# Kernel optimization log

Measured on AMD Instinct MI355X. Metric: run time of the kernel, lower is better.

Reference implementation:

```python
import jax, jax.numpy as jnp
import numpy as np

B, N, D, H, FF, K, L = 8, 4096, 128, 8, 512, 16, 2
DH = D // H
EPS = 1e-5


def setup_inputs() -> dict:
    key = jax.random.key(0)
    ks = jax.random.split(key, 32)
    s = 0.02
    inp = {
        "x": jax.random.normal(ks[0], (B, N, 8), dtype=jnp.float32),
        "xyz_w": jax.random.normal(ks[1], (D, 3), jnp.float32) * s,
        "xyz_b": jnp.zeros((D,), jnp.float32),
        "ohe_w": jax.random.normal(ks[2], (D, 5), jnp.float32) * s,
        "ohe_b": jnp.zeros((D,), jnp.float32),
        # per-layer transformer params stacked on leading L axis
        "in_proj_w": jax.random.normal(ks[3], (L, 3 * D, D), jnp.float32) * s,
        "in_proj_b": jnp.zeros((L, 3 * D), jnp.float32),
        "out_proj_w": jax.random.normal(ks[4], (L, D, D), jnp.float32) * s,
        "out_proj_b": jnp.zeros((L, D), jnp.float32),
        "ln1_w": jnp.ones((L, D), jnp.float32),
        "ln1_b": jnp.zeros((L, D), jnp.float32),
        "lin1_w": jax.random.normal(ks[5], (L, FF, D), jnp.float32) * s,
        "lin1_b": jnp.zeros((L, FF), jnp.float32),
        "lin2_w": jax.random.normal(ks[6], (L, D, FF), jnp.float32) * s,
        "lin2_b": jnp.zeros((L, D), jnp.float32),
        "ln2_w": jnp.ones((L, D), jnp.float32),
        "ln2_b": jnp.zeros((L, D), jnp.float32),
        "fc1_w": jax.random.normal(ks[7], (FF, D), jnp.float32) * s,
        "fc1_b": jnp.zeros((FF,), jnp.float32),
        "fc2_w": jax.random.normal(ks[8], (1, FF), jnp.float32) * s,
        "fc2_b": jnp.zeros((1,), jnp.float32),
    }
    return inp


def _layer_norm(x, w, b):
    m = jnp.mean(x, -1, keepdims=True)
    v = jnp.mean((x - m) ** 2, -1, keepdims=True)
    return (x - m) * jax.lax.rsqrt(v + EPS) * w + b


def _knn_attention(xyz, feat):
    # squared euclidean distances preserve top-k ordering of cdist(p=2)
    d2 = jnp.sum((xyz[:, :, None, :] - xyz[:, None, :, :]) ** 2, -1)  # [B,N,N]
    _, idx = jax.lax.top_k(-d2, K + 1)  # ascending distance
    idx = idx[..., 1:]  # drop self -> [B,N,K]
    knn = jax.vmap(lambda f, i: f[i])(feat, idx)  # [B,N,K,D]
    scale = 1.0 / np.sqrt(D)
    scores = jnp.einsum('bnd,bnkd->bnk', feat, knn) * scale
    w = jax.nn.softmax(scores, -1)
    return jnp.einsum('bnk,bnkd->bnd', w, knn)


def _mha(x, in_w, in_b, out_w, out_b):
    qkv = x @ in_w.T + in_b  # [B,N,3D]
    q, k, v = jnp.split(qkv, 3, axis=-1)
    def heads(t):
        return t.reshape(B, N, H, DH).transpose(0, 2, 1, 3)  # [B,H,N,DH]
    q, k, v = heads(q), heads(k), heads(v)
    scores = jnp.einsum('bhqd,bhkd->bhqk', q, k) / np.sqrt(DH)
    a = jax.nn.softmax(scores, -1)
    o = jnp.einsum('bhqk,bhkd->bhqd', a, v).transpose(0, 2, 1, 3).reshape(B, N, D)
    return o @ out_w.T + out_b


def reference(x, xyz_w, xyz_b, ohe_w, ohe_b, in_proj_w, in_proj_b, out_proj_w,
              out_proj_b, ln1_w, ln1_b, lin1_w, lin1_b, lin2_w, lin2_b,
              ln2_w, ln2_b, fc1_w, fc1_b, fc2_w, fc2_b):
    xyz = x[:, :, :3]
    ohe = x[:, :, 3:8]
    feat = (xyz @ xyz_w.T + xyz_b) + (ohe @ ohe_w.T + ohe_b)  # [B,N,D]
    h = _knn_attention(xyz, feat)
    # post-norm TransformerEncoder (PyTorch default, relu, no dropout at eval)
    for l in range(L):
        a = _mha(h, in_proj_w[l], in_proj_b[l], out_proj_w[l], out_proj_b[l])
        h = _layer_norm(h + a, ln1_w[l], ln1_b[l])
        f = jax.nn.relu(h @ lin1_w[l].T + lin1_b[l]) @ lin2_w[l].T + lin2_b[l]
        h = _layer_norm(h + f, ln2_w[l], ln2_b[l])
    pooled = jnp.mean(h, axis=1)  # [B,D]
    out = jax.nn.sigmoid(jax.nn.relu(pooled @ fc1_w.T + fc1_b) @ fc2_w.T + fc2_b)
    return out
```

## Files before the change

kernel.cpp:

```cpp
#include <hip/hip_runtime.h>

#define Bq 8
#define Nq 4096
#define Dq 128
#define Hq 8
#define FFq 512
#define KNNq 16
#define Lq 2
#define DHq 16
#define EPSq 1e-5f

typedef _Float16 half4 __attribute__((ext_vector_type(4)));
typedef _Float16 half2t __attribute__((ext_vector_type(2)));
typedef float v4f __attribute__((ext_vector_type(4)));

static __device__ __forceinline__ half2t pkrtz(float a, float b) {
    return __builtin_bit_cast(half2t, __builtin_amdgcn_cvt_pkrtz(a, b));
}

__global__ void wcvt_kernel(const float* __restrict__ ipw, const float* __restrict__ opw,
                            const float* __restrict__ l1w, const float* __restrict__ l2w,
                            _Float16* __restrict__ wb) {
    int i = blockIdx.x * 256 + threadIdx.x;
    float v;
    if (i < 98304) v = ipw[i];
    else if (i < 131072) v = opw[i - 98304];
    else if (i < 262144) v = l1w[i - 131072];
    else v = l2w[i - 262144];
    wb[i] = (_Float16)v;
}

__global__ void feat_kernel(const float* __restrict__ x, const float* __restrict__ xyz_w,
                            const float* __restrict__ xyz_b, const float* __restrict__ ohe_w,
                            const float* __restrict__ ohe_b, float* __restrict__ feat) {
    int i = blockIdx.x * blockDim.x + threadIdx.x;
    if (i >= Bq * Nq * Dq) return;
    int d = i & 127;
    int t = i >> 7;
    const float* xr = x + (size_t)t * 8;
    float s = xyz_b[d] + ohe_b[d];
    s += xr[0] * xyz_w[d * 3 + 0] + xr[1] * xyz_w[d * 3 + 1] + xr[2] * xyz_w[d * 3 + 2];
    s += xr[3] * ohe_w[d * 5 + 0] + xr[4] * ohe_w[d * 5 + 1] + xr[5] * ohe_w[d * 5 + 2]
       + xr[6] * ohe_w[d * 5 + 3] + xr[7] * ohe_w[d * 5 + 4];
    feat[i] = s;
}

__global__ __launch_bounds__(256) void knn_kernel(const float* __restrict__ x, int* __restrict__ idx) {
    __shared__ __attribute__((aligned(16))) float sxyz[Nq][4];
    __shared__ unsigned int md[256][16];
    int b = blockIdx.y;
    int tid = threadIdx.x;
    for (int p = tid; p < Nq; p += 256) {
        const float* xr = x + ((size_t)b * Nq + p) * 8;
        float4 v = make_float4(xr[0], xr[1], xr[2], 0.f);
        *(float4*)&sxyz[p][0] = v;
    }
    __syncthreads();
    int qi = tid >> 3;
    int part = tid & 7;
    int n = blockIdx.x * 32 + qi;
    float qx = sxyz[n][0], qy = sxyz[n][1], qz = sxyz[n][2];
    unsigned int bd[KNNq];
#pragma unroll
    for (int i = 0; i < KNNq; i++) bd[i] = 0xFFFFFFFFu;
    int j0 = part * 512;
    int rot = part * 2;
#pragma unroll 2
    for (int jj = 0; jj < 512; jj++) {
        int j = j0 + ((jj + rot) & 511);
        float4 p4 = *(const float4*)&sxyz[j][0];
        float dx = qx - p4.x, dy = qy - p4.y, dz = qz - p4.z;
        float d2 = fmaf(dx, dx, fmaf(dy, dy, dz * dz));
        unsigned int key = (__float_as_uint(d2) & 0xFFFFF000u) | (unsigned int)j;
        key = (j == n) ? 0xFFFFFFFFu : key;
#pragma unroll
        for (int i = 0; i < KNNq; i++) {
            unsigned int lo = bd[i] < key ? bd[i] : key;
            unsigned int hi = bd[i] < key ? key : bd[i];
            bd[i] = lo; key = hi;
        }
    }
#pragma unroll
    for (int i = 0; i < KNNq; i++) md[tid][i] = bd[i];
    __syncthreads();
    if (part == 0) {
        unsigned int pall = 0;
        int* op = idx + ((size_t)b * Nq + n) * KNNq;
        int base_row = qi * 8;
#pragma unroll
        for (int s = 0; s < KNNq; s++) {
            unsigned int best = 0xFFFFFFFFu; int bp = 0;
#pragma unroll
            for (int p2 = 0; p2 < 8; p2++) {
                unsigned int ptr = (pall >> (p2 * 4)) & 15u;
                unsigned int v = md[base_row + p2][ptr];
                if (v < best) { best = v; bp = p2; }
            }
            op[s] = (int)(best & 4095u);
            pall += (1u << (bp * 4));
        }
    }
}

__global__ __launch_bounds__(256, 4) void knn_attn_kernel(const float* __restrict__ feat,
                                                          const int* __restrict__ idx,
                                                          float* __restrict__ h,
                                                          _Float16* __restrict__ h16) {
    int wave = threadIdx.x >> 6;
    int lane = threadIdx.x & 63;
    int token = blockIdx.x * 4 + wave;
    int b = token >> 12;
    const float2* frow = (const float2*)(feat + (size_t)token * Dq);
    float2 f = frow[lane];
    const int* ip = idx + (size_t)token * KNNq;
    int jj[KNNq];
#pragma unroll
    for (int k = 0; k < KNNq; k++) jj[k] = ip[k];
    float2 g[KNNq];
#pragma unroll
    for (int k = 0; k < KNNq; k++)
        g[k] = ((const float2*)(feat + (((size_t)b << 12) + jj[k]) * Dq))[lane];
    float sc[KNNq];
#pragma unroll
    for (int k = 0; k < KNNq; k++) {
        float p = f.x * g[k].x + f.y * g[k].y;
#pragma unroll
        for (int m = 1; m < 64; m <<= 1) p += __shfl_xor(p, m);
        sc[k] = p * 0.088388347648318447f;
    }
    float mx = sc[0];
#pragma unroll
    for (int k = 1; k < KNNq; k++) mx = fmaxf(mx, sc[k]);
    float sum = 0.f;
#pragma unroll
    for (int k = 0; k < KNNq; k++) { sc[k] = __expf(sc[k] - mx); sum += sc[k]; }
    float inv = 1.f / sum;
    float o0 = 0.f, o1 = 0.f;
#pragma unroll
    for (int k = 0; k < KNNq; k++) { o0 += sc[k] * g[k].x; o1 += sc[k] * g[k].y; }
    o0 *= inv; o1 *= inv;
    ((float2*)(h + (size_t)token * Dq))[lane] = make_float2(o0, o1);
    ((half2t*)(h16 + (size_t)token * Dq))[lane] = pkrtz(o0, o1);
}

template <int MODE>
__global__ __launch_bounds__(256) void hgemm_kernel(const _Float16* __restrict__ A,
                                                    const _Float16* __restrict__ W,
                                                    const float* __restrict__ bias,
                                                    void* __restrict__ Cout,
                                                    int M, int Nc, int K) {
    int tid = threadIdx.x;
    int lane = tid & 63, w = tid >> 6;
    int l15 = lane & 15, l4 = lane >> 4;
    int m0 = blockIdx.y * 64 + w * 16;
    int n0 = blockIdx.x * 64;
    const _Float16* Ap = A + (size_t)(m0 + l15) * K + l4 * 4;
    const _Float16* Wp = W + (size_t)(n0 + l15) * K + l4 * 4;
    v4f acc[4] = {{0.f, 0.f, 0.f, 0.f}, {0.f, 0.f, 0.f, 0.f}, {0.f, 0.f, 0.f, 0.f}, {0.f, 0.f, 0.f, 0.f}};
    for (int ks = 0; ks < K; ks += 16) {
        half4 af = *(const half4*)(Ap + ks);
#pragma unroll
        for (int nt = 0; nt < 4; nt++) {
            half4 wf = *(const half4*)(Wp + (size_t)nt * 16 * K + ks);
            acc[nt] = __builtin_amdgcn_mfma_f32_16x16x16f16(wf, af, acc[nt], 0, 0, 0);
        }
    }
    int m = m0 + l15;
#pragma unroll
    for (int nt = 0; nt < 4; nt++) {
        int nb = n0 + nt * 16 + l4 * 4;
        float4 bv = *(const float4*)(bias + nb);
        float v0 = acc[nt][0] + bv.x, v1 = acc[nt][1] + bv.y;
        float v2 = acc[nt][2] + bv.z, v3 = acc[nt][3] + bv.w;
        if (MODE == 1) {
            v0 = fmaxf(v0, 0.f); v1 = fmaxf(v1, 0.f); v2 = fmaxf(v2, 0.f); v3 = fmaxf(v3, 0.f);
        }
        if (MODE == 0) {
            *(float4*)((float*)Cout + (size_t)m * Nc + nb) = make_float4(v0, v1, v2, v3);
        } else {
            half2t lo = pkrtz(v0, v1);
            half2t hi = pkrtz(v2, v3);
            half4 hv; hv[0] = lo[0]; hv[1] = lo[1]; hv[2] = hi[0]; hv[3] = hi[1];
            if (MODE == 1) {
                *(half4*)((_Float16*)Cout + (size_t)m * Nc + nb) = hv;
            } else {
                int n_base = n0 + nt * 16;
                int sel = n_base >> 7, hh = (n_base >> 4) & 7;
                size_t base = (size_t)sel * (64ull * Nq * 16)
                            + ((size_t)((m >> 12) * 8 + hh)) * (Nq * 16)
                            + (size_t)(m & 4095) * 16 + l4 * 4;
                *(half4*)((_Float16*)Cout + base) = hv;
            }
        }
    }
}

__global__ __launch_bounds__(256) void flash3_kernel(const _Float16* __restrict__ pk,
                                                     _Float16* __restrict__ out16) {
    __shared__ _Float16 Ks[64 * 20];
    __shared__ _Float16 Vt[16 * 68];
    int tid = threadIdx.x;
    int lane = tid & 63, w = tid >> 6;
    int bh = blockIdx.y;
    const _Float16* Qb = pk + (size_t)bh * (Nq * 16);
    const _Float16* Kb = pk + (size_t)(64 + bh) * (Nq * 16);
    const _Float16* Vb = pk + (size_t)(128 + bh) * (Nq * 16);
    int q0 = blockIdx.x * 64 + w * 16;
    int l15 = lane & 15, l4 = lane >> 4;

    half4 qf = *(const half4*)(Qb + (size_t)(q0 + l15) * 16 + l4 * 4);
#pragma unroll
    for (int i = 0; i < 4; i++) qf[i] = qf[i] * (_Float16)0.36067376f;

    v4f o = {0.f, 0.f, 0.f, 0.f};
    float lsum = 0.f;
    int sr = tid >> 2, sc = tid & 3;

    for (int kt = 0; kt < Nq / 64; kt++) {
        __syncthreads();
        {
            half4 kv = *(const half4*)(Kb + (size_t)(kt * 64 + sr) * 16 + sc * 4);
            *(half4*)(Ks + sr * 20 + sc * 4) = kv;
            half4 vv = *(const half4*)(Vb + (size_t)(kt * 64 + sr) * 16 + sc * 4);
            Vt[(sc * 4 + 0) * 68 + sr] = vv[0];
            Vt[(sc * 4 + 1) * 68 + sr] = vv[1];
            Vt[(sc * 4 + 2) * 68 + sr] = vv[2];
            Vt[(sc * 4 + 3) * 68 + sr] = vv[3];
        }
        __syncthreads();
        v4f S[4];
#pragma unroll
        for (int g = 0; g < 4; g++) {
            half4 kf = *(const half4*)(Ks + (g * 16 + l15) * 20 + l4 * 4);
            S[g] = __builtin_amdgcn_mfma_f32_16x16x16f16(kf, qf, (v4f){0.f, 0.f, 0.f, 0.f}, 0, 0, 0);
        }
        half4 P[4];
#pragma unroll
        for (int g = 0; g < 4; g++) {
            float p0 = __builtin_amdgcn_exp2f(S[g][0]);
            float p1 = __builtin_amdgcn_exp2f(S[g][1]);
            float p2 = __builtin_amdgcn_exp2f(S[g][2]);
            float p3 = __builtin_amdgcn_exp2f(S[g][3]);
            lsum += (p0 + p1) + (p2 + p3);
            half2t lo = pkrtz(p0, p1);
            half2t hi = pkrtz(p2, p3);
            P[g][0] = lo[0]; P[g][1] = lo[1]; P[g][2] = hi[0]; P[g][3] = hi[1];
        }
#pragma unroll
        for (int g = 0; g < 4; g++) {
            half4 vf = *(const half4*)(Vt + l15 * 68 + g * 16 + l4 * 4);
            o = __builtin_amdgcn_mfma_f32_16x16x16f16(vf, P[g], o, 0, 0, 0);
        }
    }
    lsum += __shfl_xor(lsum, 16);
    lsum += __shfl_xor(lsum, 32);
    float inv = 1.f / lsum;
    int row = q0 + l15;
    int b = bh >> 3, hh = bh & 7;
    half2t lo = pkrtz(o[0] * inv, o[1] * inv);
    half2t hi = pkrtz(o[2] * inv, o[3] * inv);
    half4 hv; hv[0] = lo[0]; hv[1] = lo[1]; hv[2] = hi[0]; hv[3] = hi[1];
    *(half4*)(out16 + ((size_t)(b * Nq + row)) * Dq + hh * 16 + l4 * 4) = hv;
}

__global__ __launch_bounds__(256) void add_ln_kernel(float* __restrict__ h, const float* __restrict__ res,
                                                     const float* __restrict__ w, const float* __restrict__ bta,
                                                     _Float16* __restrict__ h16) {
    int wave = threadIdx.x >> 6, lane = threadIdx.x & 63;
    int row = blockIdx.x * 4 + wave;
    float2* hr = (float2*)(h + (size_t)row * Dq);
    const float2* rr = (const float2*)(res + (size_t)row * Dq);
    float2 xv = hr[lane], rv = rr[lane];
    float x0 = xv.x + rv.x, x1 = xv.y + rv.y;
    float sm = x0 + x1;
#pragma unroll
    for (int m = 1; m < 64; m <<= 1) sm += __shfl_xor(sm, m);
    float mean = sm * (1.f / 128.f);
    float d0 = x0 - mean, d1 = x1 - mean;
    float v = d0 * d0 + d1 * d1;
#pragma unroll
    for (int m = 1; m < 64; m <<= 1) v += __shfl_xor(v, m);
    float inv = rsqrtf(v * (1.f / 128.f) + EPSq);
    float2 wv = ((const float2*)w)[lane];
    float2 bv = ((const float2*)bta)[lane];
    float y0 = d0 * inv * wv.x + bv.x;
    float y1 = d1 * inv * wv.y + bv.y;
    hr[lane] = make_float2(y0, y1);
    ((half2t*)(h16 + (size_t)row * Dq))[lane] = pkrtz(y0, y1);
}

__global__ void pool_kernel(const float* __restrict__ h, float* __restrict__ part) {
    int c = blockIdx.x, b = blockIdx.y, d = threadIdx.x;
    const float* p = h + ((size_t)b * Nq + c * 256) * Dq + d;
    float s = 0.f;
    for (int n = 0; n < 256; n++) s += p[(size_t)n * Dq];
    part[((size_t)b * 16 + c) * Dq + d] = s;
}

__global__ __launch_bounds__(512) void head_kernel(const float* __restrict__ part,
                                                   const float* __restrict__ fc1_w, const float* __restrict__ fc1_b,
                                                   const float* __restrict__ fc2_w, const float* __restrict__ fc2_b,
                                                   float* __restrict__ out) {
    __shared__ float psh[Dq];
    __shared__ float red[512];
    int b = blockIdx.x, f = threadIdx.x;
    if (f < Dq) {
        float s = 0.f;
        for (int c = 0; c < 16; c++) s += part[((size_t)b * 16 + c) * Dq + f];
        psh[f] = s * (1.f / 4096.f);
    }
    __syncthreads();
    const float* wr = fc1_w + (size_t)f * Dq;
    float s = fc1_b[f];
    for (int d = 0; d < Dq; d++) s += psh[d] * wr[d];
    red[f] = fmaxf(s, 0.f) * fc2_w[f];
    __syncthreads();
    for (int st = 256; st > 0; st >>= 1) {
        if (f < st) red[f] += red[f + st];
        __syncthreads();
    }
    if (f == 0) out[b] = 1.f / (1.f + __expf(-(red[0] + fc2_b[0])));
}

extern "C" void kernel_launch(void* const* d_in, const int* in_sizes, int n_in,
                              void* d_out, int out_size, void* d_ws, size_t ws_size,
                              hipStream_t stream) {
    const float* x        = (const float*)d_in[0];
    const float* xyz_w    = (const float*)d_in[1];
    const float* xyz_b    = (const float*)d_in[2];
    const float* ohe_w    = (const float*)d_in[3];
    const float* ohe_b    = (const float*)d_in[4];
    const float* in_proj_w  = (const float*)d_in[5];
    const float* in_proj_b  = (const float*)d_in[6];
    const float* out_proj_w = (const float*)d_in[7];
    const float* out_proj_b = (const float*)d_in[8];
    const float* ln1_w    = (const float*)d_in[9];
    const float* ln1_b    = (const float*)d_in[10];
    const float* lin1_w   = (const float*)d_in[11];
    const float* lin1_b   = (const float*)d_in[12];
    const float* lin2_w   = (const float*)d_in[13];
    const float* lin2_b   = (const float*)d_in[14];
    const float* ln2_w    = (const float*)d_in[15];
    const float* ln2_b    = (const float*)d_in[16];
    const float* fc1_w    = (const float*)d_in[17];
    const float* fc1_b    = (const float*)d_in[18];
    const float* fc2_w    = (const float*)d_in[19];
    const float* fc2_b    = (const float*)d_in[20];
    float* outp = (float*)d_out;

    char* ws = (char*)d_ws;
    size_t off = 0;
    auto alloc = [&](size_t bytes) { void* p = ws + off; off += (bytes + 255) & ~255ULL; return p; };
    float*     feat   = (float*)alloc((size_t)Bq * Nq * Dq * 4);
    float*     h      = (float*)alloc((size_t)Bq * Nq * Dq * 4);
    _Float16*  h16    = (_Float16*)alloc((size_t)Bq * Nq * Dq * 2);
    _Float16*  abuf16 = (_Float16*)alloc((size_t)Bq * Nq * Dq * 2);
    char*      bigu   = (char*)alloc((size_t)Bq * Nq * FFq * 2);
    _Float16*  wb     = (_Float16*)alloc(393216ull * 2);
    int*       idx    = (int*)alloc((size_t)Bq * Nq * KNNq * 4);
    float*     part   = (float*)alloc((size_t)Bq * 16 * Dq * 4);
    if (off > ws_size) return;
    _Float16* pkb   = (_Float16*)bigu;
    _Float16* big16 = (_Float16*)bigu;

    const _Float16* wip16 = wb;
    const _Float16* wop16 = wb + 98304;
    const _Float16* wl116 = wb + 131072;
    const _Float16* wl216 = wb + 262144;

    int M = Bq * Nq;

    wcvt_kernel<<<1536, 256, 0, stream>>>(in_proj_w, out_proj_w, lin1_w, lin2_w, wb);
    feat_kernel<<<(Bq * Nq * Dq + 255) / 256, 256, 0, stream>>>(x, xyz_w, xyz_b, ohe_w, ohe_b, feat);
    knn_kernel<<<dim3(Nq / 32, Bq), 256, 0, stream>>>(x, idx);
    knn_attn_kernel<<<M / 4, 256, 0, stream>>>(feat, idx, h, h16);

    for (int l = 0; l < Lq; l++) {
        hgemm_kernel<2><<<dim3(384 / 64, M / 64), 256, 0, stream>>>(
            h16, wip16 + (size_t)l * 384 * 128, in_proj_b + l * 384, pkb, M, 384, 128);
        flash3_kernel<<<dim3(Nq / 64, Bq * Hq), 256, 0, stream>>>(pkb, abuf16);
        hgemm_kernel<0><<<dim3(128 / 64, M / 64), 256, 0, stream>>>(
            abuf16, wop16 + (size_t)l * 128 * 128, out_proj_b + l * 128, feat, M, 128, 128);
        add_ln_kernel<<<M / 4, 256, 0, stream>>>(h, feat, ln1_w + l * 128, ln1_b + l * 128, h16);
        hgemm_kernel<1><<<dim3(512 / 64, M / 64), 256, 0, stream>>>(
            h16, wl116 + (size_t)l * 512 * 128, lin1_b + l * 512, big16, M, 512, 128);
        hgemm_kernel<0><<<dim3(128 / 64, M / 64), 256, 0, stream>>>(
            big16, wl216 + (size_t)l * 128 * 512, lin2_b + l * 128, feat, M, 128, 512);
        add_ln_kernel<<<M / 4, 256, 0, stream>>>(h, feat, ln2_w + l * 128, ln2_b + l * 128, h16);
    }

    pool_kernel<<<dim3(16, Bq), 128, 0, stream>>>(h, part);
    head_kernel<<<Bq, 512, 0, stream>>>(part, fc1_w, fc1_b, fc2_w, fc2_b, outp);
}
```

Measured before the change: 1.213 ms.

## Fuse output GEMMs with residual LayerNorm and store V pre-transposed for attention

Adds an hgemm_ln kernel in which each wave computes full 128-wide output rows and applies bias, residual add and LayerNorm in registers. This removes the separate add_ln launches and the fp32 round trip through the feat buffer. The QKV GEMM now writes V transposed to global memory, so the attention kernel reads K and V fragments straight from global without shared-memory staging or barriers. The trade-offs are strided scalar stores of V, uncached global fragment loads in the attention loop, and fewer blocks for the fused GEMM.

```diff
diff --git a/kernel.cpp b/kernel.cpp
--- a/kernel.cpp
+++ b/kernel.cpp
@@ -175,36 +175,40 @@
         if (MODE == 1) {
             v0 = fmaxf(v0, 0.f); v1 = fmaxf(v1, 0.f); v2 = fmaxf(v2, 0.f); v3 = fmaxf(v3, 0.f);
         }
-        if (MODE == 0) {
-            *(float4*)((float*)Cout + (size_t)m * Nc + nb) = make_float4(v0, v1, v2, v3);
+        half2t lo = pkrtz(v0, v1);
+        half2t hi = pkrtz(v2, v3);
+        half4 hv; hv[0] = lo[0]; hv[1] = lo[1]; hv[2] = hi[0]; hv[3] = hi[1];
+        if (MODE == 1) {
+            *(half4*)((_Float16*)Cout + (size_t)m * Nc + nb) = hv;
         } else {
-            half2t lo = pkrtz(v0, v1);
-            half2t hi = pkrtz(v2, v3);
-            half4 hv; hv[0] = lo[0]; hv[1] = lo[1]; hv[2] = hi[0]; hv[3] = hi[1];
-            if (MODE == 1) {
-                *(half4*)((_Float16*)Cout + (size_t)m * Nc + nb) = hv;
-            } else {
-                int n_base = n0 + nt * 16;
-                int sel = n_base >> 7, hh = (n_base >> 4) & 7;
+            int n_base = n0 + nt * 16;
+            int sel = n_base >> 7;
+            if (sel < 2) {
+                int hh = (n_base >> 4) & 7;
                 size_t base = (size_t)sel * (64ull * Nq * 16)
                             + ((size_t)((m >> 12) * 8 + hh)) * (Nq * 16)
                             + (size_t)(m & 4095) * 16 + l4 * 4;
                 *(half4*)((_Float16*)Cout + base) = hv;
+            } else {
+                int hh = (n_base >> 4) & 7;
+                size_t vb = 2ull * 64 * Nq * 16
+                          + ((size_t)((m >> 12) * 8 + hh)) * (16 * Nq)
+                          + (size_t)(m & 4095);
+                _Float16* vp = (_Float16*)Cout + vb + (size_t)(l4 * 4) * Nq;
+                vp[0 * Nq] = hv[0]; vp[1 * Nq] = hv[1]; vp[2 * Nq] = hv[2]; vp[3 * Nq] = hv[3];
             }
         }
     }
 }
 
-__global__ __launch_bounds__(256) void flash3_kernel(const _Float16* __restrict__ pk,
+__global__ __launch_bounds__(256) void flash4_kernel(const _Float16* __restrict__ pk,
                                                      _Float16* __restrict__ out16) {
-    __shared__ _Float16 Ks[64 * 20];
-    __shared__ _Float16 Vt[16 * 68];
     int tid = threadIdx.x;
     int lane = tid & 63, w = tid >> 6;
     int bh = blockIdx.y;
     const _Float16* Qb = pk + (size_t)bh * (Nq * 16);
     const _Float16* Kb = pk + (size_t)(64 + bh) * (Nq * 16);
-    const _Float16* Vb = pk + (size_t)(128 + bh) * (Nq * 16);
+    const _Float16* Vt = pk + 2ull * 64 * Nq * 16 + (size_t)bh * (16 * Nq);
     int q0 = blockIdx.x * 64 + w * 16;
     int l15 = lane & 15, l4 = lane >> 4;
 
@@ -214,26 +218,23 @@
 
     v4f o = {0.f, 0.f, 0.f, 0.f};
     float lsum = 0.f;
-    int sr = tid >> 2, sc = tid & 3;
-
+    const _Float16* Kfrag = Kb + (size_t)l15 * 16 + l4 * 4;
+    const _Float16* Vfrag = Vt + (size_t)l15 * Nq + l4 * 4;
+
+#pragma unroll 2
     for (int kt = 0; kt < Nq / 64; kt++) {
-        __syncthreads();
-        {
-            half4 kv = *(const half4*)(Kb + (size_t)(kt * 64 + sr) * 16 + sc * 4);
-            *(half4*)(Ks + sr * 20 + sc * 4) = kv;
-            half4 vv = *(const half4*)(Vb + (size_t)(kt * 64 + sr) * 16 + sc * 4);
-            Vt[(sc * 4 + 0) * 68 + sr] = vv[0];
-            Vt[(sc * 4 + 1) * 68 + sr] = vv[1];
-            Vt[(sc * 4 + 2) * 68 + sr] = vv[2];
-            Vt[(sc * 4 + 3) * 68 + sr] = vv[3];
-        }
-        __syncthreads();
+        half4 kf[4];
+#pragma unroll
+        for (int g = 0; g < 4; g++)
+            kf[g] = *(const half4*)(Kfrag + (size_t)(kt * 64 + g * 16) * 16);
         v4f S[4];
 #pragma unroll
-        for (int g = 0; g < 4; g++) {
-            half4 kf = *(const half4*)(Ks + (g * 16 + l15) * 20 + l4 * 4);
-            S[g] = __builtin_amdgcn_mfma_f32_16x16x16f16(kf, qf, (v4f){0.f, 0.f, 0.f, 0.f}, 0, 0, 0);
-        }
+        for (int g = 0; g < 4; g++)
+            S[g] = __builtin_amdgcn_mfma_f32_16x16x16f16(kf[g], qf, (v4f){0.f, 0.f, 0.f, 0.f}, 0, 0, 0);
+        half4 vf[4];
+#pragma unroll
+        for (int g = 0; g < 4; g++)
+            vf[g] = *(const half4*)(Vfrag + kt * 64 + g * 16);
         half4 P[4];
 #pragma unroll
         for (int g = 0; g < 4; g++) {
@@ -247,10 +248,8 @@
             P[g][0] = lo[0]; P[g][1] = lo[1]; P[g][2] = hi[0]; P[g][3] = hi[1];
         }
 #pragma unroll
-        for (int g = 0; g < 4; g++) {
-            half4 vf = *(const half4*)(Vt + l15 * 68 + g * 16 + l4 * 4);
-            o = __builtin_amdgcn_mfma_f32_16x16x16f16(vf, P[g], o, 0, 0, 0);
-        }
+        for (int g = 0; g < 4; g++)
+            o = __builtin_amdgcn_mfma_f32_16x16x16f16(vf[g], P[g], o, 0, 0, 0);
     }
     lsum += __shfl_xor(lsum, 16);
     lsum += __shfl_xor(lsum, 32);
@@ -263,30 +262,72 @@
     *(half4*)(out16 + ((size_t)(b * Nq + row)) * Dq + hh * 16 + l4 * 4) = hv;
 }
 
-__global__ __launch_bounds__(256) void add_ln_kernel(float* __restrict__ h, const float* __restrict__ res,
-                                                     const float* __restrict__ w, const float* __restrict__ bta,
-                                                     _Float16* __restrict__ h16) {
-    int wave = threadIdx.x >> 6, lane = threadIdx.x & 63;
-    int row = blockIdx.x * 4 + wave;
-    float2* hr = (float2*)(h + (size_t)row * Dq);
-    const float2* rr = (const float2*)(res + (size_t)row * Dq);
-    float2 xv = hr[lane], rv = rr[lane];
-    float x0 = xv.x + rv.x, x1 = xv.y + rv.y;
-    float sm = x0 + x1;
-#pragma unroll
-    for (int m = 1; m < 64; m <<= 1) sm += __shfl_xor(sm, m);
-    float mean = sm * (1.f / 128.f);
-    float d0 = x0 - mean, d1 = x1 - mean;
-    float v = d0 * d0 + d1 * d1;
-#pragma unroll
-    for (int m = 1; m < 64; m <<= 1) v += __shfl_xor(v, m);
-    float inv = rsqrtf(v * (1.f / 128.f) + EPSq);
-    float2 wv = ((const float2*)w)[lane];
-    float2 bv = ((const float2*)bta)[lane];
-    float y0 = d0 * inv * wv.x + bv.x;
-    float y1 = d1 * inv * wv.y + bv.y;
-    hr[lane] = make_float2(y0, y1);
-    ((half2t*)(h16 + (size_t)row * Dq))[lane] = pkrtz(y0, y1);
+__global__ __launch_bounds__(256) void hgemm_ln_kernel(const _Float16* __restrict__ A,
+                                                       const _Float16* __restrict__ W,
+                                                       const float* __restrict__ bias,
+                                                       const float* __restrict__ lnw,
+                                                       const float* __restrict__ lnb,
+                                                       float* __restrict__ h,
+                                                       _Float16* __restrict__ h16,
+                                                       int K) {
+    int tid = threadIdx.x;
+    int lane = tid & 63, w = tid >> 6;
+    int l15 = lane & 15, l4 = lane >> 4;
+    int m0 = blockIdx.x * 64 + w * 16;
+    const _Float16* Ap = A + (size_t)(m0 + l15) * K + l4 * 4;
+    const _Float16* Wp = W + (size_t)l15 * K + l4 * 4;
+    v4f acc[8] = {};
+    for (int ks = 0; ks < K; ks += 16) {
+        half4 af = *(const half4*)(Ap + ks);
+#pragma unroll
+        for (int nt = 0; nt < 8; nt++) {
+            half4 wf = *(const half4*)(Wp + (size_t)nt * 16 * K + ks);
+            acc[nt] = __builtin_amdgcn_mfma_f32_16x16x16f16(wf, af, acc[nt], 0, 0, 0);
+        }
+    }
+    int m = m0 + l15;
+    float x[8][4];
+    float psum = 0.f;
+#pragma unroll
+    for (int nt = 0; nt < 8; nt++) {
+        int nb = nt * 16 + l4 * 4;
+        float4 bv = *(const float4*)(bias + nb);
+        float4 hv = *(const float4*)(h + (size_t)m * Dq + nb);
+        x[nt][0] = acc[nt][0] + bv.x + hv.x;
+        x[nt][1] = acc[nt][1] + bv.y + hv.y;
+        x[nt][2] = acc[nt][2] + bv.z + hv.z;
+        x[nt][3] = acc[nt][3] + bv.w + hv.w;
+        psum += (x[nt][0] + x[nt][1]) + (x[nt][2] + x[nt][3]);
+    }
+    psum += __shfl_xor(psum, 16);
+    psum += __shfl_xor(psum, 32);
+    float mean = psum * (1.f / 128.f);
+    float vsum = 0.f;
+#pragma unroll
+    for (int nt = 0; nt < 8; nt++)
+#pragma unroll
+        for (int r = 0; r < 4; r++) {
+            x[nt][r] -= mean;
+            vsum += x[nt][r] * x[nt][r];
+        }
+    vsum += __shfl_xor(vsum, 16);
+    vsum += __shfl_xor(vsum, 32);
+    float inv = rsqrtf(vsum * (1.f / 128.f) + EPSq);
+#pragma unroll
+    for (int nt = 0; nt < 8; nt++) {
+        int nb = nt * 16 + l4 * 4;
+        float4 wv = *(const float4*)(lnw + nb);
+        float4 bb = *(const float4*)(lnb + nb);
+        float y0 = x[nt][0] * inv * wv.x + bb.x;
+        float y1 = x[nt][1] * inv * wv.y + bb.y;
+        float y2 = x[nt][2] * inv * wv.z + bb.z;
+        float y3 = x[nt][3] * inv * wv.w + bb.w;
+        *(float4*)(h + (size_t)m * Dq + nb) = make_float4(y0, y1, y2, y3);
+        half2t lo = pkrtz(y0, y1);
+        half2t hi = pkrtz(y2, y3);
+        half4 hv2; hv2[0] = lo[0]; hv2[1] = lo[1]; hv2[2] = hi[0]; hv2[3] = hi[1];
+        *(half4*)(h16 + (size_t)m * Dq + nb) = hv2;
+    }
 }
 
 __global__ void pool_kernel(const float* __restrict__ h, float* __restrict__ part) {
@@ -378,15 +419,15 @@
     for (int l = 0; l < Lq; l++) {
         hgemm_kernel<2><<<dim3(384 / 64, M / 64), 256, 0, stream>>>(
             h16, wip16 + (size_t)l * 384 * 128, in_proj_b + l * 384, pkb, M, 384, 128);
-        flash3_kernel<<<dim3(Nq / 64, Bq * Hq), 256, 0, stream>>>(pkb, abuf16);
-        hgemm_kernel<0><<<dim3(128 / 64, M / 64), 256, 0, stream>>>(
-            abuf16, wop16 + (size_t)l * 128 * 128, out_proj_b + l * 128, feat, M, 128, 128);
-        add_ln_kernel<<<M / 4, 256, 0, stream>>>(h, feat, ln1_w + l * 128, ln1_b + l * 128, h16);
+        flash4_kernel<<<dim3(Nq / 64, Bq * Hq), 256, 0, stream>>>(pkb, abuf16);
+        hgemm_ln_kernel<<<M / 64, 256, 0, stream>>>(
+            abuf16, wop16 + (size_t)l * 128 * 128, out_proj_b + l * 128,
+            ln1_w + l * 128, ln1_b + l * 128, h, h16, 128);
         hgemm_kernel<1><<<dim3(512 / 64, M / 64), 256, 0, stream>>>(
             h16, wl116 + (size_t)l * 512 * 128, lin1_b + l * 512, big16, M, 512, 128);
-        hgemm_kernel<0><<<dim3(128 / 64, M / 64), 256, 0, stream>>>(
-            big16, wl216 + (size_t)l * 128 * 512, lin2_b + l * 128, feat, M, 128, 512);
-        add_ln_kernel<<<M / 4, 256, 0, stream>>>(h, feat, ln2_w + l * 128, ln2_b + l * 128, h16);
+        hgemm_ln_kernel<<<M / 64, 256, 0, stream>>>(
+            big16, wl216 + (size_t)l * 128 * 512, lin2_b + l * 128,
+            ln2_w + l * 128, ln2_b + l * 128, h, h16, 512);
     }
 
     pool_kernel<<<dim3(16, Bq), 128, 0, stream>>>(h, part);
```

Measured after the change: 1.923 ms. 1.59x slower.
